# Optimization experiments

Hardware: AMD Instinct MI355X
Metric: run time of the kernel (lower is better)

Reference implementation:

```python
import math
import jax, jax.numpy as jnp
import numpy as np

B, H, S, D = 2, 16, 2048, 64
NEG = -1000000000.0


def setup_inputs() -> dict:
    key = jax.random.key(0)
    kq, kk, kv = jax.random.split(key, 3)
    q = jax.random.normal(kq, (B, H, S, D), dtype=jnp.float32)
    k = jax.random.normal(kk, (B, H, S, D), dtype=jnp.float32)
    v = jax.random.normal(kv, (B, H, S, D), dtype=jnp.float32)
    attention_mask = jnp.ones((B, S), dtype=jnp.float32)
    return {"q": q, "k": k, "v": v, "attention_mask": attention_mask}


def reference(q, k, v, attention_mask):
    head_dim = q.shape[-1]
    scaling = 1.0 / math.sqrt(head_dim)
    # scores: [B, H, S, S]
    scores = jnp.einsum("bhqd,bhkd->bhqk", q, k) * scaling
    seq_len = q.shape[-2]
    # causal mask: upper triangle (excluding diag) gets large negative
    causal_mask = jnp.triu(jnp.full((seq_len, seq_len), NEG, dtype=scores.dtype), k=1)
    scores = scores + causal_mask[None, None, :, :]
    # additive attention mask: [B,1,1,S]
    add_mask = (1.0 - attention_mask)[:, None, None, :] * NEG
    scores = scores + add_mask
    weights = jax.nn.softmax(scores, axis=-1)  # dropout p=0.0 -> identity
    out = jnp.einsum("bhqk,bhkd->bhqd", weights, v)
    return out
```

## Files before the change

### kernel.cpp

```cpp
#include <hip/hip_runtime.h>

typedef _Float16 half8 __attribute__((ext_vector_type(8)));
typedef float f32x4 __attribute__((ext_vector_type(4)));

#define MFMA_F16 __builtin_amdgcn_mfma_f32_16x16x32_f16

constexpr int Sc = 2048, Dc = 64;
constexpr int QBLK = 128, KVBLK = 64;
constexpr float LOG2E = 1.4426950408889634f;
constexpr float SCALE_LOG2E = 0.125f * LOG2E;
constexpr float NEGBIG = -1.0e9f;

constexpr size_t WS_MADD = 65536;
constexpr size_t WS_KIMG = 524288;
constexpr size_t WS_VIMG = WS_KIMG + (size_t)1024 * 8192;

#define J(q, a, b) ((uint32_t)(q) | ((uint32_t)(a) << 8) | ((uint32_t)(b) << 16))
__device__ const uint32_t JOBS[40] = {
    J(15,0,8),  J(15,8,16), J(15,16,24), J(15,24,32),
    J(14,7,15), J(14,22,30),J(11,0,8),   J(11,8,16),
    J(13,0,7),  J(14,15,22),J(14,0,7),   J(3,0,8),
    J(7,8,16),  J(7,0,8),   J(10,14,22), J(11,16,24),
    J(13,7,14), J(13,14,21),J(13,21,28), J(12,6,13),
    J(12,19,26),J(10,0,7),  J(10,7,14),  J(9,6,13),
    J(9,13,20), J(6,0,7),   J(6,7,14),   J(12,0,6),
    J(12,13,19),J(9,0,6),   J(8,0,6),    J(8,6,12),
    J(8,12,18), J(5,0,6),   J(5,6,12),   J(2,0,6),
    J(4,0,5),   J(4,5,10),  J(1,0,4),    J(0,0,2)
};

__global__ __launch_bounds__(256, 4)
void prep(const float* __restrict__ K, const float* __restrict__ V,
          const float* __restrict__ AM, float* __restrict__ O,
          float* __restrict__ ws)
{
    const int bid = blockIdx.x;
    const int t   = threadIdx.x;

    if (bid >= 1024) {
        const int zb = bid - 1024;
        float4* O4 = (float4*)O;
        const float4 z = {0.f, 0.f, 0.f, 0.f};
        #pragma unroll
        for (int i = 0; i < 4; ++i) O4[(size_t)zb * 1024 + i * 256 + t] = z;
        if (zb < 16) {
            float4* L4 = (float4*)ws;
            #pragma unroll
            for (int i = 0; i < 4; ++i) L4[(size_t)zb * 1024 + i * 256 + t] = z;
        }
        return;
    }

    __shared__ float Vlds[64][65];
    const int bh  = bid & 31;
    const int kvt = bid >> 5;
    const size_t base = (size_t)bh * Sc * Dc + (size_t)kvt * KVBLK * Dc;
    _Float16* Kimg = (_Float16*)((char*)ws + WS_KIMG) + ((size_t)(bh * 32 + kvt) << 12);
    _Float16* Vimg = (_Float16*)((char*)ws + WS_VIMG) + ((size_t)(bh * 32 + kvt) << 12);

    #pragma unroll
    for (int i = 0; i < 4; ++i) {
        const int r = (t >> 4) + 16 * i, c = (t & 15) * 4;
        float4 v = *(const float4*)(V + base + (size_t)r * Dc + c);
        Vlds[r][c] = v.x; Vlds[r][c+1] = v.y; Vlds[r][c+2] = v.z; Vlds[r][c+3] = v.w;
    }

    #pragma unroll
    for (int ss = 0; ss < 2; ++ss) {
        const int s = t + 256 * ss;
        const int nt = s >> 7, cc = (s >> 6) & 1, hi = (s >> 4) & 3, l16 = s & 15;
        const float* kp = K + base + (size_t)(nt * 16 + l16) * Dc + cc * 32 + hi * 8;
        float4 a = *(const float4*)kp;
        float4 b = *(const float4*)(kp + 4);
        half8 h = { (_Float16)a.x, (_Float16)a.y, (_Float16)a.z, (_Float16)a.w,
                    (_Float16)b.x, (_Float16)b.y, (_Float16)b.z, (_Float16)b.w };
        *(half8*)(Kimg + (size_t)s * 8) = h;
    }
    __syncthreads();

    #pragma unroll
    for (int ss = 0; ss < 2; ++ss) {
        const int s = t + 256 * ss;
        const int dt = s >> 7, cc = (s >> 6) & 1, hi = (s >> 4) & 3, l16 = s & 15;
        const int d = dt * 16 + l16;
        half8 h;
        #pragma unroll
        for (int j = 0; j < 8; ++j) {
            const int ks  = cc * 32 + hi * 8 + j;
            const int key = ((ks >> 5) << 5) | (((ks >> 2) & 1) << 4)
                          | (((ks >> 3) & 3) << 2) | (ks & 3);
            h[j] = (_Float16)Vlds[key][d];
        }
        *(half8*)(Vimg + (size_t)s * 8) = h;
    }

    if ((bh & 15) == 0 && t < 64) {
        const size_t idx = (size_t)(bh >> 4) * Sc + kvt * 64 + t;
        (ws + WS_MADD)[idx] = (1.0f - AM[idx]) * (NEGBIG * LOG2E);
    }
}

__global__ __launch_bounds__(256, 4)
void sdpa_p1(const float* __restrict__ Q, float* __restrict__ Oacc,
             float* __restrict__ ws)
{
    const float* maddp = ws + WS_MADD;
    const _Float16* Kimg = (const _Float16*)((const char*)ws + WS_KIMG);
    const _Float16* Vimg = (const _Float16*)((const char*)ws + WS_VIMG);
    float* Lp = ws;

    const int bid = blockIdx.x;
    const int bh  = bid & 31;
    const uint32_t job = JOBS[bid >> 5];
    const int qt  = job & 255;
    const int kv0 = (job >> 8) & 255;
    const int kv1 = (job >> 16) & 255;
    const int b   = bh >> 4;
    const int qb  = qt * QBLK;

    const int t    = threadIdx.x;
    const int w    = t >> 6;
    const int lane = t & 63;
    const int l16  = lane & 15;
    const int hi   = lane >> 4;
    const int hi4  = hi * 4;

    const size_t base  = (size_t)bh * Sc * Dc;
    const size_t tbase = (size_t)bh * 32;

    half8 qfrag[2][2];
    #pragma unroll
    for (int g = 0; g < 2; ++g) {
        const float* qp = Q + base + (size_t)(qb + w * 32 + g * 16 + l16) * Dc + hi * 8;
        #pragma unroll
        for (int cc = 0; cc < 2; ++cc) {
            float4 x0 = *(const float4*)(qp + cc * 32);
            float4 x1 = *(const float4*)(qp + cc * 32 + 4);
            qfrag[g][cc] = (half8){
                (_Float16)(x0.x * SCALE_LOG2E), (_Float16)(x0.y * SCALE_LOG2E),
                (_Float16)(x0.z * SCALE_LOG2E), (_Float16)(x0.w * SCALE_LOG2E),
                (_Float16)(x1.x * SCALE_LOG2E), (_Float16)(x1.y * SCALE_LOG2E),
                (_Float16)(x1.z * SCALE_LOG2E), (_Float16)(x1.w * SCALE_LOG2E) };
        }
    }

    f32x4 o[2][4];
    #pragma unroll
    for (int g = 0; g < 2; ++g)
        #pragma unroll
        for (int dt = 0; dt < 4; ++dt) o[g][dt] = (f32x4){0.f, 0.f, 0.f, 0.f};
    float lacc[2] = {0.f, 0.f};

    for (int kvt = kv0; kvt < kv1; ++kvt) {
        const _Float16* Kt = Kimg + ((tbase + kvt) << 12) + lane * 8;
        const _Float16* Vt = Vimg + ((tbase + kvt) << 12) + lane * 8;
        const int kvb = kvt * KVBLK;

        half8 kf[8];
        #pragma unroll
        for (int i = 0; i < 8; ++i) kf[i] = *(const half8*)(Kt + i * 512);

        f32x4 st[2][4];
        #pragma unroll
        for (int g = 0; g < 2; ++g)
            #pragma unroll
            for (int nt = 0; nt < 4; ++nt) st[g][nt] = (f32x4){0.f, 0.f, 0.f, 0.f};
        #pragma unroll
        for (int nt = 0; nt < 4; ++nt)
            #pragma unroll
            for (int cc = 0; cc < 2; ++cc)
                #pragma unroll
                for (int g = 0; g < 2; ++g)
                    st[g][nt] = MFMA_F16(kf[nt * 2 + cc], qfrag[g][cc], st[g][nt], 0, 0, 0);

        half8 vfA[4];
        #pragma unroll
        for (int i = 0; i < 4; ++i) vfA[i] = *(const half8*)(Vt + i * 512);

        #pragma unroll
        for (int nt = 0; nt < 4; ++nt) {
            const f32x4 mr = *(const f32x4*)(maddp + (size_t)b * Sc + kvb + nt * 16 + hi4);
            #pragma unroll
            for (int g = 0; g < 2; ++g)
                #pragma unroll
                for (int r = 0; r < 4; ++r) st[g][nt][r] += mr[r];
        }
        if (kvt >= 2 * qt) {
            #pragma unroll
            for (int g = 0; g < 2; ++g) {
                const int qrow = qb + w * 32 + g * 16 + l16;
                #pragma unroll
                for (int nt = 0; nt < 4; ++nt)
                    #pragma unroll
                    for (int r = 0; r < 4; ++r)
                        if (kvb + nt * 16 + hi4 + r > qrow) st[g][nt][r] = NEGBIG;
            }
        }

        #pragma unroll
        for (int g = 0; g < 2; ++g)
            #pragma unroll
            for (int nt = 0; nt < 4; ++nt)
                #pragma unroll
                for (int r = 0; r < 4; ++r) {
                    const float p = exp2f(st[g][nt][r]);
                    lacc[g] += p;
                    st[g][nt][r] = p;
                }

        half8 pa[2][2];
        #pragma unroll
        for (int g = 0; g < 2; ++g)
            #pragma unroll
            for (int cc = 0; cc < 2; ++cc)
                #pragma unroll
                for (int jj = 0; jj < 8; ++jj)
                    pa[g][cc][jj] = (_Float16)st[g][2 * cc + (jj >> 2)][jj & 3];

        half8 vfB[4];
        #pragma unroll
        for (int i = 0; i < 4; ++i) vfB[i] = *(const half8*)(Vt + (4 + i) * 512);

        #pragma unroll
        for (int dt = 0; dt < 2; ++dt)
            #pragma unroll
            for (int cc = 0; cc < 2; ++cc)
                #pragma unroll
                for (int g = 0; g < 2; ++g)
                    o[g][dt] = MFMA_F16(pa[g][cc], vfA[dt * 2 + cc], o[g][dt], 0, 0, 0);
        #pragma unroll
        for (int dt = 2; dt < 4; ++dt)
            #pragma unroll
            for (int cc = 0; cc < 2; ++cc)
                #pragma unroll
                for (int g = 0; g < 2; ++g)
                    o[g][dt] = MFMA_F16(pa[g][cc], vfB[(dt - 2) * 2 + cc], o[g][dt], 0, 0, 0);
    }

    #pragma unroll
    for (int g = 0; g < 2; ++g) {
        float la = lacc[g];
        la += __shfl_xor(la, 16);
        la += __shfl_xor(la, 32);
        if (hi == 0)
            unsafeAtomicAdd(&Lp[(size_t)bh * Sc + qb + w * 32 + g * 16 + l16], la);
        float* op = Oacc + base + (size_t)(qb + w * 32 + g * 16 + hi4) * Dc + l16;
        #pragma unroll
        for (int r = 0; r < 4; ++r)
            #pragma unroll
            for (int dt = 0; dt < 4; ++dt)
                unsafeAtomicAdd(&op[(size_t)r * Dc + dt * 16], o[g][dt][r]);
    }
}

__global__ __launch_bounds__(256)
void sdpa_norm(float* __restrict__ O, const float* __restrict__ L)
{
    const int i = blockIdx.x * 256 + threadIdx.x;
    float4* o4 = (float4*)O;
    float4 v = o4[i];
    const float inv = 1.0f / L[i >> 4];
    v.x *= inv; v.y *= inv; v.z *= inv; v.w *= inv;
    o4[i] = v;
}

extern "C" void kernel_launch(void* const* d_in, const int* in_sizes, int n_in,
                              void* d_out, int out_size, void* d_ws, size_t ws_size,
                              hipStream_t stream)
{
    const float* q  = (const float*)d_in[0];
    const float* k  = (const float*)d_in[1];
    const float* v  = (const float*)d_in[2];
    const float* am = (const float*)d_in[3];
    float* out = (float*)d_out;
    float* wsf = (float*)d_ws;

    prep    <<<2048, 256, 0, stream>>>(k, v, am, out, wsf);
    sdpa_p1 <<<1280, 256, 0, stream>>>(q, out, wsf);
    sdpa_norm<<<4096, 256, 0, stream>>>(out, wsf);
}
```

Baseline: 171.1 us.

## Shrink query tile to 64 rows and split causal KV range into computed chunks

Each block now handles 64 query rows (one 16-row group per wave) instead of 128, and the causal KV range is split into 1–4 chunks chosen by a closed-form mapping. This replaces the hand-tuned job table and doubles the grid to 2560 blocks, aiming for better load balance and occupancy. The cost is half the K/V reuse per block, so each K/V tile is loaded twice as often, and there are more atomic partial-sum writes to O and L.

New measurement: 158.0 us. 7.7% less time.

```diff
diff --git a/kernel.cpp b/kernel.cpp
--- a/kernel.cpp
+++ b/kernel.cpp
@@ -6,7 +6,7 @@
 #define MFMA_F16 __builtin_amdgcn_mfma_f32_16x16x32_f16
 
 constexpr int Sc = 2048, Dc = 64;
-constexpr int QBLK = 128, KVBLK = 64;
+constexpr int KVBLK = 64;
 constexpr float LOG2E = 1.4426950408889634f;
 constexpr float SCALE_LOG2E = 0.125f * LOG2E;
 constexpr float NEGBIG = -1.0e9f;
@@ -14,20 +14,6 @@
 constexpr size_t WS_MADD = 65536;
 constexpr size_t WS_KIMG = 524288;
 constexpr size_t WS_VIMG = WS_KIMG + (size_t)1024 * 8192;
-
-#define J(q, a, b) ((uint32_t)(q) | ((uint32_t)(a) << 8) | ((uint32_t)(b) << 16))
-__device__ const uint32_t JOBS[40] = {
-    J(15,0,8),  J(15,8,16), J(15,16,24), J(15,24,32),
-    J(14,7,15), J(14,22,30),J(11,0,8),   J(11,8,16),
-    J(13,0,7),  J(14,15,22),J(14,0,7),   J(3,0,8),
-    J(7,8,16),  J(7,0,8),   J(10,14,22), J(11,16,24),
-    J(13,7,14), J(13,14,21),J(13,21,28), J(12,6,13),
-    J(12,19,26),J(10,0,7),  J(10,7,14),  J(9,6,13),
-    J(9,13,20), J(6,0,7),   J(6,7,14),   J(12,0,6),
-    J(12,13,19),J(9,0,6),   J(8,0,6),    J(8,6,12),
-    J(8,12,18), J(5,0,6),   J(5,6,12),   J(2,0,6),
-    J(4,0,5),   J(4,5,10),  J(1,0,4),    J(0,0,2)
-};
 
 __global__ __launch_bounds__(256, 4)
 void prep(const float* __restrict__ K, const float* __restrict__ V,
@@ -111,12 +97,21 @@
 
     const int bid = blockIdx.x;
     const int bh  = bid & 31;
-    const uint32_t job = JOBS[bid >> 5];
-    const int qt  = job & 255;
-    const int kv0 = (job >> 8) & 255;
-    const int kv1 = (job >> 16) & 255;
-    const int b   = bh >> 4;
-    const int qb  = qt * QBLK;
+    const int c0  = (bid >> 5) & 7;
+    const int kk  = bid >> 8;
+    const int j   = ((kk & 1) ? (7 - c0) : c0) + 8 * kk;
+
+    int qt, c, nc;
+    if (j < 8)       { qt = j;                   c = 0;              nc = 1; }
+    else if (j < 24) { qt = 8 + ((j - 8) >> 1);  c = (j - 8) & 1;    nc = 2; }
+    else if (j < 48) { qt = 16 + (j - 24) / 3;   c = (j - 24) % 3;   nc = 3; }
+    else             { qt = 24 + ((j - 48) >> 2); c = (j - 48) & 3;  nc = 4; }
+    const int n   = qt + 1;
+    const int kv0 = c * n / nc;
+    const int kv1 = (c + 1) * n / nc;
+
+    const int b  = bh >> 4;
+    const int qb = qt * 64;
 
     const int t    = threadIdx.x;
     const int w    = t >> 6;
@@ -128,15 +123,14 @@
     const size_t base  = (size_t)bh * Sc * Dc;
     const size_t tbase = (size_t)bh * 32;
 
-    half8 qfrag[2][2];
-    #pragma unroll
-    for (int g = 0; g < 2; ++g) {
-        const float* qp = Q + base + (size_t)(qb + w * 32 + g * 16 + l16) * Dc + hi * 8;
+    half8 qfrag[2];
+    {
+        const float* qp = Q + base + (size_t)(qb + w * 16 + l16) * Dc + hi * 8;
         #pragma unroll
         for (int cc = 0; cc < 2; ++cc) {
             float4 x0 = *(const float4*)(qp + cc * 32);
             float4 x1 = *(const float4*)(qp + cc * 32 + 4);
-            qfrag[g][cc] = (half8){
+            qfrag[cc] = (half8){
                 (_Float16)(x0.x * SCALE_LOG2E), (_Float16)(x0.y * SCALE_LOG2E),
                 (_Float16)(x0.z * SCALE_LOG2E), (_Float16)(x0.w * SCALE_LOG2E),
                 (_Float16)(x1.x * SCALE_LOG2E), (_Float16)(x1.y * SCALE_LOG2E),
@@ -144,12 +138,12 @@
         }
     }
 
-    f32x4 o[2][4];
-    #pragma unroll
-    for (int g = 0; g < 2; ++g)
-        #pragma unroll
-        for (int dt = 0; dt < 4; ++dt) o[g][dt] = (f32x4){0.f, 0.f, 0.f, 0.f};
-    float lacc[2] = {0.f, 0.f};
+    f32x4 o[4];
+    #pragma unroll
+    for (int dt = 0; dt < 4; ++dt) o[dt] = (f32x4){0.f, 0.f, 0.f, 0.f};
+    float lacc = 0.f;
+
+    const int qg = qb + w * 16 + l16;
 
     for (int kvt = kv0; kvt < kv1; ++kvt) {
         const _Float16* Kt = Kimg + ((tbase + kvt) << 12) + lane * 8;
@@ -160,18 +154,14 @@
         #pragma unroll
         for (int i = 0; i < 8; ++i) kf[i] = *(const half8*)(Kt + i * 512);
 
-        f32x4 st[2][4];
-        #pragma unroll
-        for (int g = 0; g < 2; ++g)
-            #pragma unroll
-            for (int nt = 0; nt < 4; ++nt) st[g][nt] = (f32x4){0.f, 0.f, 0.f, 0.f};
-        #pragma unroll
-        for (int nt = 0; nt < 4; ++nt)
+        f32x4 st[4];
+        #pragma unroll
+        for (int nt = 0; nt < 4; ++nt) {
+            st[nt] = (f32x4){0.f, 0.f, 0.f, 0.f};
             #pragma unroll
             for (int cc = 0; cc < 2; ++cc)
-                #pragma unroll
-                for (int g = 0; g < 2; ++g)
-                    st[g][nt] = MFMA_F16(kf[nt * 2 + cc], qfrag[g][cc], st[g][nt], 0, 0, 0);
+                st[nt] = MFMA_F16(kf[nt * 2 + cc], qfrag[cc], st[nt], 0, 0, 0);
+        }
 
         half8 vfA[4];
         #pragma unroll
@@ -181,76 +171,59 @@
         for (int nt = 0; nt < 4; ++nt) {
             const f32x4 mr = *(const f32x4*)(maddp + (size_t)b * Sc + kvb + nt * 16 + hi4);
             #pragma unroll
-            for (int g = 0; g < 2; ++g)
-                #pragma unroll
-                for (int r = 0; r < 4; ++r) st[g][nt][r] += mr[r];
-        }
-        if (kvt >= 2 * qt) {
-            #pragma unroll
-            for (int g = 0; g < 2; ++g) {
-                const int qrow = qb + w * 32 + g * 16 + l16;
-                #pragma unroll
-                for (int nt = 0; nt < 4; ++nt)
-                    #pragma unroll
-                    for (int r = 0; r < 4; ++r)
-                        if (kvb + nt * 16 + hi4 + r > qrow) st[g][nt][r] = NEGBIG;
-            }
-        }
-
-        #pragma unroll
-        for (int g = 0; g < 2; ++g)
+            for (int r = 0; r < 4; ++r) st[nt][r] += mr[r];
+        }
+        if (kvt == qt) {
             #pragma unroll
             for (int nt = 0; nt < 4; ++nt)
                 #pragma unroll
-                for (int r = 0; r < 4; ++r) {
-                    const float p = exp2f(st[g][nt][r]);
-                    lacc[g] += p;
-                    st[g][nt][r] = p;
-                }
-
-        half8 pa[2][2];
-        #pragma unroll
-        for (int g = 0; g < 2; ++g)
+                for (int r = 0; r < 4; ++r)
+                    if (kvb + nt * 16 + hi4 + r > qg) st[nt][r] = NEGBIG;
+        }
+
+        #pragma unroll
+        for (int nt = 0; nt < 4; ++nt)
+            #pragma unroll
+            for (int r = 0; r < 4; ++r) {
+                const float p = exp2f(st[nt][r]);
+                lacc += p;
+                st[nt][r] = p;
+            }
+
+        half8 pa[2];
+        #pragma unroll
+        for (int cc = 0; cc < 2; ++cc)
+            #pragma unroll
+            for (int jj = 0; jj < 8; ++jj)
+                pa[cc][jj] = (_Float16)st[2 * cc + (jj >> 2)][jj & 3];
+
+        half8 vfB[4];
+        #pragma unroll
+        for (int i = 0; i < 4; ++i) vfB[i] = *(const half8*)(Vt + (4 + i) * 512);
+
+        #pragma unroll
+        for (int dt = 0; dt < 2; ++dt)
             #pragma unroll
             for (int cc = 0; cc < 2; ++cc)
-                #pragma unroll
-                for (int jj = 0; jj < 8; ++jj)
-                    pa[g][cc][jj] = (_Float16)st[g][2 * cc + (jj >> 2)][jj & 3];
-
-        half8 vfB[4];
-        #pragma unroll
-        for (int i = 0; i < 4; ++i) vfB[i] = *(const half8*)(Vt + (4 + i) * 512);
-
-        #pragma unroll
-        for (int dt = 0; dt < 2; ++dt)
+                o[dt] = MFMA_F16(pa[cc], vfA[dt * 2 + cc], o[dt], 0, 0, 0);
+        #pragma unroll
+        for (int dt = 2; dt < 4; ++dt)
             #pragma unroll
             for (int cc = 0; cc < 2; ++cc)
-                #pragma unroll
-                for (int g = 0; g < 2; ++g)
-                    o[g][dt] = MFMA_F16(pa[g][cc], vfA[dt * 2 + cc], o[g][dt], 0, 0, 0);
-        #pragma unroll
-        for (int dt = 2; dt < 4; ++dt)
-            #pragma unroll
-            for (int cc = 0; cc < 2; ++cc)
-                #pragma unroll
-                for (int g = 0; g < 2; ++g)
-                    o[g][dt] = MFMA_F16(pa[g][cc], vfB[(dt - 2) * 2 + cc], o[g][dt], 0, 0, 0);
-    }
-
-    #pragma unroll
-    for (int g = 0; g < 2; ++g) {
-        float la = lacc[g];
-        la += __shfl_xor(la, 16);
-        la += __shfl_xor(la, 32);
-        if (hi == 0)
-            unsafeAtomicAdd(&Lp[(size_t)bh * Sc + qb + w * 32 + g * 16 + l16], la);
-        float* op = Oacc + base + (size_t)(qb + w * 32 + g * 16 + hi4) * Dc + l16;
-        #pragma unroll
-        for (int r = 0; r < 4; ++r)
-            #pragma unroll
-            for (int dt = 0; dt < 4; ++dt)
-                unsafeAtomicAdd(&op[(size_t)r * Dc + dt * 16], o[g][dt][r]);
-    }
+                o[dt] = MFMA_F16(pa[cc], vfB[(dt - 2) * 2 + cc], o[dt], 0, 0, 0);
+    }
+
+    lacc += __shfl_xor(lacc, 16);
+    lacc += __shfl_xor(lacc, 32);
+    if (hi == 0)
+        unsafeAtomicAdd(&Lp[(size_t)bh * Sc + qb + w * 16 + l16], lacc);
+
+    float* op = Oacc + base + (size_t)(qb + w * 16 + hi4) * Dc + l16;
+    #pragma unroll
+    for (int r = 0; r < 4; ++r)
+        #pragma unroll
+        for (int dt = 0; dt < 4; ++dt)
+            unsafeAtomicAdd(&op[(size_t)r * Dc + dt * 16], o[dt][r]);
 }
 
 __global__ __launch_bounds__(256)
@@ -276,6 +249,6 @@
     float* wsf = (float*)d_ws;
 
     prep    <<<2048, 256, 0, stream>>>(k, v, am, out, wsf);
-    sdpa_p1 <<<1280, 256, 0, stream>>>(q, out, wsf);
+    sdpa_p1 <<<2560, 256, 0, stream>>>(q, out, wsf);
     sdpa_norm<<<4096, 256, 0, stream>>>(out, wsf);
 }
```
